# Kernel optimization log

Hardware: AMD Instinct MI355X
Metric: run time of the kernel (lower is better)

The kernel has to match this reference:

```python
import jax, jax.numpy as jnp
import numpy as np

# MLA (multi-head latent attention) config
DIM = 1024
HEADS = 16
DIM_HEAD = DIM // HEADS          # 64
LATENT = DIM // 4                # 256, compressed KV latent dim
SCALE = DIM_HEAD ** -0.5


def setup_inputs() -> dict:
    key = jax.random.key(0)
    ks = jax.random.split(key, 8)
    B, S = 2, 2048
    init = lambda k, shape, fan_in: jax.random.normal(k, shape, jnp.float32) * (fan_in ** -0.5)
    return {
        "x":  jax.random.normal(ks[0], (B, S, DIM), jnp.float32),
        "Wq": init(ks[1], (DIM, DIM), DIM),
        "bq": jnp.zeros((DIM,), jnp.float32),
        "Wl": init(ks[2], (DIM, LATENT), DIM),      # down-projection to compressed KV latent
        "bl": jnp.zeros((LATENT,), jnp.float32),
        "Wk": init(ks[3], (LATENT, DIM), LATENT),   # latent -> per-head keys
        "bk": jnp.zeros((DIM,), jnp.float32),
        "Wv": init(ks[4], (LATENT, DIM), LATENT),   # latent -> per-head values
        "bv": jnp.zeros((DIM,), jnp.float32),
        "Wo": init(ks[5], (DIM, DIM), DIM),         # Attention.to_out
        "bo": jnp.zeros((DIM,), jnp.float32),
    }


def reference(x, Wq, bq, Wl, bl, Wk, bk, Wv, bv, Wo, bo):
    B, S, D = x.shape
    H, Dh = HEADS, DIM_HEAD
    # query projection
    q = (x @ Wq + bq).reshape(B, S, H, Dh)
    # compressed KV latent (this is what would be cached; kv_cache=None here)
    latent = x @ Wl + bl                              # [B, S, LATENT]
    k = (latent @ Wk + bk).reshape(B, S, H, Dh)
    v = (latent @ Wv + bv).reshape(B, S, H, Dh)
    # attention
    scores = jnp.einsum('bihd,bjhd->bhij', q, k) * SCALE   # [B, H, S, S]
    attn = jax.nn.softmax(scores, axis=-1)
    out = jnp.einsum('bhij,bjhd->bihd', attn, v).reshape(B, S, D)
    # dropout(p=0) is identity; output projection
    out = out @ Wo + bo
    return out
```

## Files before the change

kernel.cpp:

```cpp
#include <hip/hip_runtime.h>


typedef _Float16 half8  __attribute__((ext_vector_type(8)));
typedef _Float16 half4  __attribute__((ext_vector_type(4)));
typedef __fp16   fp16x2 __attribute__((ext_vector_type(2)));
typedef float    floatx4 __attribute__((ext_vector_type(4)));
typedef float    floatx16 __attribute__((ext_vector_type(16)));

#if __has_builtin(__builtin_amdgcn_exp2f)
#define EXP2F(x) __builtin_amdgcn_exp2f(x)
#else
#define EXP2F(x) exp2f(x)
#endif

__global__ __launch_bounds__(256) void prep(
    const float* __restrict__ x,
    const float* __restrict__ Wq, const float* __restrict__ Wl,
    const float* __restrict__ Wk, const float* __restrict__ Wv,
    const float* __restrict__ Wo,
    _Float16* __restrict__ xh,
    _Float16* __restrict__ Bt1, _Float16* __restrict__ Bt2,
    _Float16* __restrict__ Wot)
{
    const int t = threadIdx.x;
    if (blockIdx.z == 5) {
        size_t base = ((size_t)(blockIdx.y * 32 + blockIdx.x) * 256 + t) * 16;
#pragma unroll
        for (int it = 0; it < 4; ++it) {
            floatx4 v = *(const floatx4*)(x + base + it * 4);
            *(half4*)(xh + base + it * 4) = __builtin_convertvector(v, half4);
        }
        return;
    }
    const float* src; _Float16* dst; int K, N;
    switch (blockIdx.z) {
        case 0:  src = Wq; dst = Bt1;                 K = 1024; N = 1024; break;
        case 1:  src = Wl; dst = Bt1 + 1024 * 1024;   K = 1024; N = 256;  break;
        case 2:  src = Wk; dst = Bt2;                 K = 256;  N = 1024; break;
        case 3:  src = Wv; dst = Bt2 + 1024 * 256;    K = 256;  N = 1024; break;
        default: src = Wo; dst = Wot;                 K = 1024; N = 1024; break;
    }
    const int n0 = blockIdx.x * 32, k0 = blockIdx.y * 32;
    if (n0 >= N || k0 >= K) return;
    __shared__ _Float16 tile[32][33];
    const int tx = t & 31, ty = t >> 5;
#pragma unroll
    for (int i = 0; i < 4; ++i)
        tile[ty + 8 * i][tx] = (_Float16)src[(size_t)(k0 + ty + 8 * i) * N + n0 + tx];
    __syncthreads();
#pragma unroll
    for (int i = 0; i < 4; ++i)
        dst[(size_t)(n0 + ty + 8 * i) * K + k0 + tx] = tile[tx][ty + 8 * i];
}

template <int MODE>
__global__ __launch_bounds__(256) void gemm_fused(
    const _Float16* __restrict__ A, const _Float16* __restrict__ Bt,
    const float* __restrict__ bias0, const float* __restrict__ bias1,
    void* __restrict__ out0, void* __restrict__ out1,
    int N, int K)
{
    __shared__ _Float16 As[128 * 64];
    __shared__ _Float16 Bs[64 * 64];
    __shared__ _Float16 Tt[(MODE == 1) ? 64 * 136 : 1];
    const int t = threadIdx.x;
    const int lane = t & 63, w = t >> 6;
    const int quad = lane >> 4, low = lane & 15;
    const int row0 = blockIdx.y * 128, col0 = blockIdx.x * 64;
    const int wm = (w >> 1) * 64, wn = (w & 1) * 32;

    floatx4 acc[4][2];
    const floatx4 z4 = {0.f, 0.f, 0.f, 0.f};
#pragma unroll
    for (int i = 0; i < 4; ++i)
#pragma unroll
        for (int j = 0; j < 2; ++j) acc[i][j] = z4;

    const int srow8 = lane >> 3;
    const int sslot = lane & 7;
    const int fswz = (low & 7);

    for (int k0 = 0; k0 < K; k0 += 64) {
        __syncthreads();
#pragma unroll
        for (int c = 0; c < 4; ++c) {
            const int chunk = w * 4 + c;
            const int row = chunk * 8 + srow8;
            const int g = sslot ^ (row & 7);
            const _Float16* gp = A + (size_t)(row0 + row) * K + k0 + g * 8;
            __builtin_amdgcn_global_load_lds(
                (const __attribute__((address_space(1))) void*)gp,
                (__attribute__((address_space(3))) void*)(As + chunk * 512), 16, 0, 0);
        }
#pragma unroll
        for (int c = 0; c < 2; ++c) {
            const int chunk = w * 2 + c;
            const int row = chunk * 8 + srow8;
            const int g = sslot ^ (row & 7);
            const _Float16* gp = Bt + (size_t)(col0 + row) * K + k0 + g * 8;
            __builtin_amdgcn_global_load_lds(
                (const __attribute__((address_space(1))) void*)gp,
                (__attribute__((address_space(3))) void*)(Bs + chunk * 512), 16, 0, 0);
        }
        __syncthreads();

#pragma unroll
        for (int kk = 0; kk < 2; ++kk) {
            const int slot = ((4 * kk + quad) ^ fswz) << 3;
            half8 a[4], b[2];
#pragma unroll
            for (int i = 0; i < 4; ++i)
                a[i] = *(const half8*)(As + (wm + i * 16 + low) * 64 + slot);
#pragma unroll
            for (int j = 0; j < 2; ++j)
                b[j] = *(const half8*)(Bs + (wn + j * 16 + low) * 64 + slot);
#pragma unroll
            for (int i = 0; i < 4; ++i)
#pragma unroll
                for (int j = 0; j < 2; ++j)
                    acc[i][j] = __builtin_amdgcn_mfma_f32_16x16x32_f16(a[i], b[j], acc[i][j], 0, 0, 0);
        }
    }

    if (MODE == 1 && col0 >= 1024) {
        const int hh = (col0 - 1024) >> 6;
        const int bb = row0 >> 11;
        const int tok0 = row0 & 2047;
#pragma unroll
        for (int i = 0; i < 4; ++i)
#pragma unroll
            for (int j = 0; j < 2; ++j) {
                const int lc = wn + j * 16 + low;
                float bv = bias1[hh * 64 + lc];
                half4 ph;
#pragma unroll
                for (int r = 0; r < 4; ++r) ph[r] = (_Float16)(acc[i][j][r] + bv);
                *(half4*)(&Tt[lc * 136 + wm + i * 16 + quad * 4]) = ph;
            }
        __syncthreads();
        _Float16* vb = (_Float16*)out1 + ((size_t)(bb * 16 + hh) * 64) * 2048;
#pragma unroll
        for (int it = 0; it < 4; ++it) {
            const int e = t + 256 * it;
            const int d = e >> 4, tk = (e & 15) * 8;
            half8 val = *(const half8*)(&Tt[d * 136 + tk]);
            *(half8*)(vb + (size_t)d * 2048 + tok0 + tk) = val;
        }
        return;
    }

#pragma unroll
    for (int i = 0; i < 4; ++i) {
#pragma unroll
        for (int j = 0; j < 2; ++j) {
            const int col = col0 + wn + j * 16 + low;
            const int rbase = row0 + wm + i * 16 + quad * 4;
            if (MODE == 2) {
                const float bv = bias0[col];
#pragma unroll
                for (int r = 0; r < 4; ++r)
                    ((float*)out0)[(size_t)(rbase + r) * 1024 + col] = acc[i][j][r] + bv;
            } else if (col < 1024) {
                float bv = bias0[col];
#pragma unroll
                for (int r = 0; r < 4; ++r) {
                    float val = acc[i][j][r] + bv;
                    if (MODE == 0) val *= 0.180336880f;
                    ((_Float16*)out0)[(size_t)(rbase + r) * 1024 + col] = (_Float16)val;
                }
            } else {
                const int c2 = col - 1024;
                float bv = bias1[c2];
#pragma unroll
                for (int r = 0; r < 4; ++r)
                    ((_Float16*)out1)[(size_t)(rbase + r) * 256 + c2] =
                        (_Float16)(acc[i][j][r] + bv);
            }
        }
    }
}

__device__ __forceinline__ unsigned pk2(float a, float b) {
    union { fp16x2 h; unsigned u; } x;
    x.h = __builtin_amdgcn_cvt_pkrtz(a, b);
    return x.u;
}

__global__ __launch_bounds__(256) void mla_attn(
    const _Float16* __restrict__ qp,
    const _Float16* __restrict__ kk,
    const _Float16* __restrict__ vt,
    _Float16* __restrict__ Op0, _Float16* __restrict__ Op1,
    float* __restrict__ lp)
{
    constexpr int S = 2048;
    __shared__ _Float16 Ks[64][76];
    __shared__ _Float16 Vs[64][76];

    const int t = threadIdx.x, lane = t & 63, w = t >> 6;
    const int l31 = lane & 31, hi = lane >> 5;
    const int q0 = blockIdx.x * 128;
    const int b = blockIdx.y >> 4, h = blockIdx.y & 15;
    const int split = blockIdx.z;

    half8 qf[4];
#pragma unroll
    for (int ks = 0; ks < 4; ++ks)
        qf[ks] = *(const half8*)(qp +
            (size_t)(b * S + q0 + w * 32 + l31) * 1024 + h * 64 + ks * 16 + hi * 8);

    floatx16 oa[2];
#pragma unroll
    for (int nd = 0; nd < 2; ++nd)
#pragma unroll
        for (int r = 0; r < 16; ++r) oa[nd][r] = 0.f;
    float ls = 0.f;

    const _Float16* kbase = kk + (size_t)(b * S) * 1024 + h * 64;
    const _Float16* vbase = vt + (size_t)(b * 16 + h) * 64 * 2048;

    const int jbeg = split * 1024, jend = jbeg + 1024;
    for (int j0 = jbeg; j0 < jend; j0 += 64) {
        __syncthreads();
#pragma unroll
        for (int p = 0; p < 2; ++p) {
            const int c = p * 256 + t;
            const int r = c >> 3, g = c & 7;
            *(half8*)(&Ks[r][g * 8]) =
                *(const half8*)(kbase + (size_t)(j0 + r) * 1024 + g * 8);
            *(half8*)(&Vs[r][g * 8]) =
                *(const half8*)(vbase + (size_t)r * 2048 + j0 + g * 8);
        }
        __syncthreads();

        floatx16 sc[2];
#pragma unroll
        for (int jb = 0; jb < 2; ++jb)
#pragma unroll
            for (int r = 0; r < 16; ++r) sc[jb][r] = -4.f;

        __builtin_amdgcn_s_setprio(1);
#pragma unroll
        for (int jb = 0; jb < 2; ++jb)
#pragma unroll
            for (int ks = 0; ks < 4; ++ks) {
                half8 kf = *(const half8*)(&Ks[jb * 32 + l31][ks * 16 + hi * 8]);
                sc[jb] = __builtin_amdgcn_mfma_f32_32x32x16_f16(kf, qf[ks], sc[jb], 0, 0, 0);
            }
        __builtin_amdgcn_s_setprio(0);

        half8 pfrag[2][2];
#pragma unroll
        for (int jb = 0; jb < 2; ++jb) {
#pragma unroll
            for (int r = 0; r < 16; ++r) {
                sc[jb][r] = EXP2F(sc[jb][r]);
                ls += sc[jb][r];
            }
#pragma unroll
            for (int kb = 0; kb < 2; ++kb) {
                unsigned a0 = pk2(sc[jb][8 * kb + 0], sc[jb][8 * kb + 1]);
                unsigned a1 = pk2(sc[jb][8 * kb + 2], sc[jb][8 * kb + 3]);
                unsigned b0 = pk2(sc[jb][8 * kb + 4], sc[jb][8 * kb + 5]);
                unsigned b1 = pk2(sc[jb][8 * kb + 6], sc[jb][8 * kb + 7]);
                asm("v_permlane32_swap_b32 %0, %1" : "+v"(a0), "+v"(b0));
                asm("v_permlane32_swap_b32 %0, %1" : "+v"(a1), "+v"(b1));
                union { unsigned u[4]; half8 h; } pu;
                pu.u[0] = a0; pu.u[1] = a1; pu.u[2] = b0; pu.u[3] = b1;
                pfrag[jb][kb] = pu.h;
            }
        }

        __builtin_amdgcn_s_setprio(1);
#pragma unroll
        for (int jb = 0; jb < 2; ++jb)
#pragma unroll
            for (int kb = 0; kb < 2; ++kb)
#pragma unroll
                for (int nd = 0; nd < 2; ++nd) {
                    half8 vf = *(const half8*)(
                        &Vs[nd * 32 + l31][jb * 32 + kb * 16 + hi * 8]);
                    oa[nd] = __builtin_amdgcn_mfma_f32_32x32x16_f16(pfrag[jb][kb], vf, oa[nd], 0, 0, 0);
                }
        __builtin_amdgcn_s_setprio(0);
    }

    float l2 = ls + __shfl_xor(ls, 32);
    if (hi == 0)
        lp[split * 65536 + (b * 16 + h) * 2048 + q0 + w * 32 + l31] = l2;

    _Float16* op = split ? Op1 : Op0;
#pragma unroll
    for (int nd = 0; nd < 2; ++nd)
#pragma unroll
        for (int r = 0; r < 16; ++r) {
            const int qrow = (r & 3) + 8 * (r >> 2) + 4 * hi;
            op[(size_t)(b * S + q0 + w * 32 + qrow) * 1024 +
               h * 64 + nd * 32 + l31] = (_Float16)oa[nd][r];
        }
}

__global__ __launch_bounds__(256) void attn_combine(
    const _Float16* __restrict__ O0, const _Float16* __restrict__ O1,
    const float* __restrict__ lp, _Float16* __restrict__ att)
{
    size_t idx = ((size_t)blockIdx.x * 256 + threadIdx.x) * 8;
    int row = (int)(idx >> 10), c = (int)(idx & 1023);
    int b = row >> 11, qq = row & 2047, h = c >> 6;
    int li = (b * 16 + h) * 2048 + qq;
    float inv = 1.f / (lp[li] + lp[65536 + li]);
    half8 a = *(const half8*)(O0 + idx);
    half8 bb = *(const half8*)(O1 + idx);
    half8 o;
#pragma unroll
    for (int r = 0; r < 8; ++r)
        o[r] = (_Float16)(((float)a[r] + (float)bb[r]) * inv);
    *(half8*)(att + idx) = o;
}

extern "C" void kernel_launch(void* const* d_in, const int* in_sizes, int n_in,
                              void* d_out, int out_size, void* d_ws, size_t ws_size,
                              hipStream_t stream) {
    const float* x  = (const float*)d_in[0];
    const float* Wq = (const float*)d_in[1];
    const float* bq = (const float*)d_in[2];
    const float* Wl = (const float*)d_in[3];
    const float* bl = (const float*)d_in[4];
    const float* Wk = (const float*)d_in[5];
    const float* bk = (const float*)d_in[6];
    const float* Wv = (const float*)d_in[7];
    const float* bv = (const float*)d_in[8];
    const float* Wo = (const float*)d_in[9];
    const float* bo = (const float*)d_in[10];
    float* out = (float*)d_out;

    _Float16* p   = (_Float16*)d_ws;
    _Float16* xh  = p; p += 4194304;
    _Float16* qh  = p; p += 4194304;
    _Float16* kh  = p; p += 4194304;
    _Float16* vtb = p; p += 4194304;
    _Float16* ah  = p; p += 4194304;
    _Float16* lat = p; p += 1048576;
    _Float16* Bt1 = p; p += 1310720;
    _Float16* Bt2 = p; p += 524288;
    _Float16* Wot = p; p += 1048576;

    prep<<<dim3(32, 32, 6), 256, 0, stream>>>(x, Wq, Wl, Wk, Wv, Wo, xh, Bt1, Bt2, Wot);

    gemm_fused<0><<<dim3(20, 32), 256, 0, stream>>>(
        xh, Bt1, bq, bl, qh, lat, 1280, 1024);
    gemm_fused<1><<<dim3(32, 32), 256, 0, stream>>>(
        lat, Bt2, bk, bv, kh, vtb, 2048, 256);
    mla_attn<<<dim3(16, 32, 2), 256, 0, stream>>>(qh, kh, vtb, ah, xh, (float*)lat);
    attn_combine<<<2048, 256, 0, stream>>>(ah, xh, (const float*)lat, kh);
    gemm_fused<2><<<dim3(16, 32), 256, 0, stream>>>(
        kh, Wot, bo, nullptr, out, nullptr, 1024, 1024);
}
```

Before: 204.5 us.

## Double-buffer K/V tiles in LDS with register prefetch in attention loop

```diff
diff --git a/kernel.cpp b/kernel.cpp
--- a/kernel.cpp
+++ b/kernel.cpp
@@ -186,7 +186,7 @@
     return x.u;
 }
 
-__global__ __launch_bounds__(256) void mla_attn(
+__global__ __launch_bounds__(256, 4) void mla_attn(
     const _Float16* __restrict__ qp,
     const _Float16* __restrict__ kk,
     const _Float16* __restrict__ vt,
@@ -194,8 +194,8 @@
     float* __restrict__ lp)
 {
     constexpr int S = 2048;
-    __shared__ _Float16 Ks[64][76];
-    __shared__ _Float16 Vs[64][76];
+    __shared__ _Float16 Ks[2][64][76];
+    __shared__ _Float16 Vs[2][64][76];
 
     const int t = threadIdx.x, lane = t & 63, w = t >> 6;
     const int l31 = lane & 31, hi = lane >> 5;
@@ -219,19 +219,33 @@
     const _Float16* kbase = kk + (size_t)(b * S) * 1024 + h * 64;
     const _Float16* vbase = vt + (size_t)(b * 16 + h) * 64 * 2048;
 
+    const int r0 = t >> 3, g8 = (t & 7) * 8;
+    const int r1 = 32 + r0;
+
     const int jbeg = split * 1024, jend = jbeg + 1024;
+
+    half8 kr0, kr1, vr0, vr1;
+    kr0 = *(const half8*)(kbase + (size_t)(jbeg + r0) * 1024 + g8);
+    kr1 = *(const half8*)(kbase + (size_t)(jbeg + r1) * 1024 + g8);
+    vr0 = *(const half8*)(vbase + (size_t)r0 * 2048 + jbeg + g8);
+    vr1 = *(const half8*)(vbase + (size_t)r1 * 2048 + jbeg + g8);
+    *(half8*)(&Ks[0][r0][g8]) = kr0;
+    *(half8*)(&Ks[0][r1][g8]) = kr1;
+    *(half8*)(&Vs[0][r0][g8]) = vr0;
+    *(half8*)(&Vs[0][r1][g8]) = vr1;
+    {
+        const int jn = jbeg + 64;
+        kr0 = *(const half8*)(kbase + (size_t)(jn + r0) * 1024 + g8);
+        kr1 = *(const half8*)(kbase + (size_t)(jn + r1) * 1024 + g8);
+        vr0 = *(const half8*)(vbase + (size_t)r0 * 2048 + jn + g8);
+        vr1 = *(const half8*)(vbase + (size_t)r1 * 2048 + jn + g8);
+    }
+    __syncthreads();
+
+    int cur = 0;
     for (int j0 = jbeg; j0 < jend; j0 += 64) {
-        __syncthreads();
-#pragma unroll
-        for (int p = 0; p < 2; ++p) {
-            const int c = p * 256 + t;
-            const int r = c >> 3, g = c & 7;
-            *(half8*)(&Ks[r][g * 8]) =
-                *(const half8*)(kbase + (size_t)(j0 + r) * 1024 + g * 8);
-            *(half8*)(&Vs[r][g * 8]) =
-                *(const half8*)(vbase + (size_t)r * 2048 + j0 + g * 8);
-        }
-        __syncthreads();
+        const _Float16 (*Kc)[76] = Ks[cur];
+        const _Float16 (*Vc)[76] = Vs[cur];
 
         floatx16 sc[2];
 #pragma unroll
@@ -239,15 +253,13 @@
 #pragma unroll
             for (int r = 0; r < 16; ++r) sc[jb][r] = -4.f;
 
-        __builtin_amdgcn_s_setprio(1);
 #pragma unroll
         for (int jb = 0; jb < 2; ++jb)
 #pragma unroll
             for (int ks = 0; ks < 4; ++ks) {
-                half8 kf = *(const half8*)(&Ks[jb * 32 + l31][ks * 16 + hi * 8]);
+                half8 kf = *(const half8*)(&Kc[jb * 32 + l31][ks * 16 + hi * 8]);
                 sc[jb] = __builtin_amdgcn_mfma_f32_32x32x16_f16(kf, qf[ks], sc[jb], 0, 0, 0);
             }
-        __builtin_amdgcn_s_setprio(0);
 
         half8 pfrag[2][2];
 #pragma unroll
@@ -271,7 +283,6 @@
             }
         }
 
-        __builtin_amdgcn_s_setprio(1);
 #pragma unroll
         for (int jb = 0; jb < 2; ++jb)
 #pragma unroll
@@ -279,10 +290,26 @@
 #pragma unroll
                 for (int nd = 0; nd < 2; ++nd) {
                     half8 vf = *(const half8*)(
-                        &Vs[nd * 32 + l31][jb * 32 + kb * 16 + hi * 8]);
+                        &Vc[nd * 32 + l31][jb * 32 + kb * 16 + hi * 8]);
                     oa[nd] = __builtin_amdgcn_mfma_f32_32x32x16_f16(pfrag[jb][kb], vf, oa[nd], 0, 0, 0);
                 }
-        __builtin_amdgcn_s_setprio(0);
+
+        if (j0 + 64 < jend) {
+            const int nxt = cur ^ 1;
+            *(half8*)(&Ks[nxt][r0][g8]) = kr0;
+            *(half8*)(&Ks[nxt][r1][g8]) = kr1;
+            *(half8*)(&Vs[nxt][r0][g8]) = vr0;
+            *(half8*)(&Vs[nxt][r1][g8]) = vr1;
+            if (j0 + 128 < jend) {
+                const int jn = j0 + 128;
+                kr0 = *(const half8*)(kbase + (size_t)(jn + r0) * 1024 + g8);
+                kr1 = *(const half8*)(kbase + (size_t)(jn + r1) * 1024 + g8);
+                vr0 = *(const half8*)(vbase + (size_t)r0 * 2048 + jn + g8);
+                vr1 = *(const half8*)(vbase + (size_t)r1 * 2048 + jn + g8);
+            }
+        }
+        __syncthreads();
+        cur ^= 1;
     }
 
     float l2 = ls + __shfl_xor(ls, 32);
```

Result: slower. 284.7 us (+39.2%).
